# Kernel optimization log

Measured on AMD Instinct MI355X. Metric: run time of the kernel, lower is better.

The kernel has to match this reference:

```python
import jax, jax.numpy as jnp
import numpy as np

D_MODEL = 256
N_HEADS = 8
EPS = 1e-6


def _split_heads(x, h=N_HEADS):
    # (b, n, D) -> (b, h, n, d)
    b, n, D = x.shape
    return x.reshape(b, n, h, D // h).transpose(0, 2, 1, 3)


def _merge_heads(x):
    # (b, h, n, d) -> (b, n, D)
    b, h, n, d = x.shape
    return x.transpose(0, 2, 1, 3).reshape(b, n, h * d)


def _hodge_diag(x, q, k, inv):
    # diagonal discrete Hodge operator: per-position scalar from q.k
    d = q.shape[-1]
    hval = jnp.einsum('bhmd,bhmd->bhm', q, k) / jnp.sqrt(jnp.asarray(d, x.dtype))
    if inv:
        hval = 1.0 / (hval + EPS)
    return hval[..., None] * x


def _forward(x_v, x_e, x_f, d_0, d_1,
             W_vq, W_vk, W_eq, W_ek, W_einvq, W_einvk, W_ev, W_fq, W_fk, W_o):
    # project + split into heads: (b, h, n, d_head)
    v_Q = _split_heads(x_v @ W_vq)
    v_K = _split_heads(x_v @ W_vk)
    e_Q = _split_heads(x_e @ W_eq)
    e_K = _split_heads(x_e @ W_ek)
    e_inv_Q = _split_heads(x_e @ W_einvq)
    e_inv_K = _split_heads(x_e @ W_einvk)
    e_V = _split_heads(x_e @ W_ev)
    f_Q = _split_heads(x_f @ W_fq)
    f_K = _split_heads(x_f @ W_fk)

    # --- up-Laplacian branch: *1^{-1} d_1^T *2 d_1 ---
    _x = e_V
    _x = jnp.einsum('bkm,bhmd->bhkd', d_1, _x)          # d_1 @ x   (edges -> faces)
    _x = _hodge_diag(_x, f_Q, f_K, inv=False)            # *2
    _x = jnp.einsum('bkm,bhkd->bhmd', d_1, _x)           # d_1^T @ x (faces -> edges)
    _x = _hodge_diag(_x, e_inv_Q, e_inv_K, inv=False)    # *1^{-1} (as diag ops, inv=False)

    # --- down-Laplacian branch: d_0 *0^{-1} d_0^T *1 ---
    _y = _hodge_diag(e_V, e_Q, e_K, inv=False)           # *1
    _y = jnp.einsum('bmn,bhmd->bhnd', d_0, _y)           # d_0^T @ y (edges -> vertices)
    _y = _hodge_diag(_y, v_Q, v_K, inv=True)             # *0^{-1} (reciprocal)
    _y = jnp.einsum('bmn,bhnd->bhmd', d_0, _y)           # d_0 @ y  (vertices -> edges)

    out = _merge_heads(_y + _x)                          # (b, m, D)
    return out @ W_o


def setup_inputs() -> dict:
    key = jax.random.key(0)
    ks = jax.random.split(key, 16)
    b, n, m, k, D = 2, 2048, 6144, 4096, D_MODEL
    s = 1.0 / np.sqrt(D)
    inp = {
        'x_v': jax.random.normal(ks[0], (b, n, D), jnp.float32),
        'x_e': jax.random.normal(ks[1], (b, m, D), jnp.float32),
        'x_f': jax.random.normal(ks[2], (b, k, D), jnp.float32),
        'd_0': jax.random.normal(ks[3], (b, m, n), jnp.float32) * 0.02,
        'd_1': jax.random.normal(ks[4], (b, k, m), jnp.float32) * 0.02,
    }
    names = ['W_vq', 'W_vk', 'W_eq', 'W_ek', 'W_einvq', 'W_einvk', 'W_ev', 'W_fq', 'W_fk', 'W_o']
    for i, nm in enumerate(names):
        inp[nm] = jax.random.normal(ks[5 + i], (D, D), jnp.float32) * s
    return inp


def reference(x_v, x_e, x_f, d_0, d_1,
              W_vq, W_vk, W_eq, W_ek, W_einvq, W_einvk, W_ev, W_fq, W_fk, W_o):
    return _forward(x_v, x_e, x_f, d_0, d_1,
                    W_vq, W_vk, W_eq, W_ek, W_einvq, W_einvk, W_ev, W_fq, W_fk, W_o)
```

## Files before the change

### kernel.cpp

```cpp
#include <hip/hip_runtime.h>
#include <hip/hip_bf16.h>
#include <cstdint>
#include <cstddef>


typedef __attribute__((ext_vector_type(4))) float f32x4;
typedef __attribute__((ext_vector_type(4))) unsigned short u16x4;
typedef __attribute__((ext_vector_type(8))) unsigned short u16x8;
typedef __attribute__((ext_vector_type(8))) __bf16 bf16x8;

static __device__ __forceinline__ unsigned short f2bf(float f) {
  uint32_t u = __builtin_bit_cast(uint32_t, f);
  uint32_t r = (u + 0x7FFFu + ((u >> 16) & 1u)) >> 16;
  return (unsigned short)r;
}
static __device__ __forceinline__ float bf2f(unsigned short h) {
  return __builtin_bit_cast(float, (uint32_t)h << 16);
}

struct GJob {
  const unsigned short* Ah; const unsigned short* Bh; float* C;
  int K, ldA, ldB, S, gx, gy;
  long long sA, sB, sC;
};

template <bool XFAST>
__global__ __launch_bounds__(256) void gemm_dual(GJob j0, GJob j1, int nb0) {
  const bool first = (int)blockIdx.x < nb0;
  GJob J = first ? j0 : j1;
  const int b = first ? blockIdx.x : blockIdx.x - nb0;
  const int per = J.gx * J.gy;
  const int z = b / per;
  const int wid = b - z * per;
  const int batch = z / J.S, split = z - batch * J.S;
  const unsigned short* Ah = J.Ah + (long long)batch * J.sA;
  const unsigned short* Bh = J.Bh + (long long)batch * J.sB;
  float* C = J.C + (long long)z * J.sC;

  const int nwg = per;
  const int q = nwg >> 3, r = nwg & 7;
  const int xcd = wid & 7, posn = wid >> 3;
  const int swz = (xcd < r ? xcd * (q + 1) : r * (q + 1) + (xcd - r) * q) + posn;
  int mt, nt;
  if constexpr (XFAST) { mt = swz % J.gx; nt = swz / J.gx; }
  else                 { mt = swz / J.gy; nt = swz - mt * J.gy; }
  const int m0 = mt * 128, n0 = nt * 128;
  const int NC = J.gy << 7;
  const int kLen = J.K / J.S, k0base = split * kLen;

  __shared__ unsigned short lds[2][128][40];

  const int t = threadIdx.x;
  const int w4 = t >> 6, lane = t & 63;
  const int wr = w4 >> 1, wc = w4 & 1;
  const int lr = lane & 15, kq = lane >> 4;
  const int rowV = t >> 2, c8V = (t & 3) * 8;

  u16x8 rA[2], rB[2];
  auto LOAD = [&](int kb) {
    #pragma unroll
    for (int a = 0; a < 2; ++a) {
      rA[a] = *(const u16x8*)(Ah + (size_t)(m0 + rowV + 64 * a) * J.ldA + kb + c8V);
      rB[a] = *(const u16x8*)(Bh + (size_t)(n0 + rowV + 64 * a) * J.ldB + kb + c8V);
    }
  };
  auto STORE = [&]() {
    #pragma unroll
    for (int a = 0; a < 2; ++a) {
      *(u16x8*)&lds[0][rowV + 64 * a][c8V] = rA[a];
      *(u16x8*)&lds[1][rowV + 64 * a][c8V] = rB[a];
    }
  };

  f32x4 acc[4][4] = {};
  LOAD(k0base);
  for (int kk = 0; kk < kLen; kk += 32) {
    STORE();
    __syncthreads();
    if (kk + 32 < kLen) LOAD(k0base + kk + 32);

    bf16x8 ah[4], bh[4];
    #pragma unroll
    for (int i = 0; i < 4; ++i) {
      ah[i] = __builtin_bit_cast(bf16x8, *(const u16x8*)&lds[0][wr * 64 + i * 16 + lr][kq * 8]);
      bh[i] = __builtin_bit_cast(bf16x8, *(const u16x8*)&lds[1][wc * 64 + i * 16 + lr][kq * 8]);
    }
    #pragma unroll
    for (int i = 0; i < 4; ++i)
      #pragma unroll
      for (int j = 0; j < 4; ++j)
        acc[i][j] = __builtin_amdgcn_mfma_f32_16x16x32_bf16(ah[i], bh[j], acc[i][j], 0, 0, 0);
    __syncthreads();
  }

  #pragma unroll
  for (int i = 0; i < 4; ++i)
    #pragma unroll
    for (int j = 0; j < 4; ++j) {
      float* cp = C + (size_t)(m0 + wr * 64 + i * 16 + kq * 4) * NC + n0 + wc * 64 + j * 16 + lr;
      #pragma unroll
      for (int qq = 0; qq < 4; ++qq) cp[(size_t)qq * NC] = acc[i][j][qq];
    }
}

template <bool SPLIT>
__global__ __launch_bounds__(256) void gemm_ws(
    const float* __restrict__ Af,
    const unsigned short* __restrict__ Bh, const unsigned short* __restrict__ Bl,
    float* __restrict__ C, int K, int ldA, int ldB,
    long long sA, long long sB, long long sC) {
  const int gx = gridDim.x, gy = gridDim.y;
  const int nwg = gx * gy;
  const int wid = blockIdx.x + gx * blockIdx.y;
  const int q = nwg >> 3, r = nwg & 7;
  const int xcd = wid & 7, posn = wid >> 3;
  const int swz = (xcd < r ? xcd * (q + 1) : r * (q + 1) + (xcd - r) * q) + posn;
  const int mt = swz / gy;
  const int m0 = mt * 128, n0 = (swz - mt * gy) * 128;
  const int NC = gy << 7;

  constexpr int NBUF = SPLIT ? 4 : 2;
  __shared__ unsigned short lds[NBUF][128][40];

  const int t = threadIdx.x;
  const int w4 = t >> 6, lane = t & 63;
  const int wr = w4 >> 1, wc = w4 & 1;
  const int lr = lane & 15, kq = lane >> 4;
  const int rowA8 = t >> 3, qdA = (t & 7) * 4;
  const int rowV = t >> 2, c8V = (t & 3) * 8;

  f32x4 rAf[4];
  u16x8 rBh[2], rBl[2];

  auto LOAD = [&](int kb) {
    #pragma unroll
    for (int a = 0; a < 4; ++a)
      rAf[a] = *(const f32x4*)(Af + (size_t)(m0 + rowA8 + 32 * a) * ldA + kb + qdA);
    #pragma unroll
    for (int a = 0; a < 2; ++a) {
      rBh[a] = *(const u16x8*)(Bh + (size_t)(n0 + rowV + 64 * a) * ldB + kb + c8V);
      if constexpr (SPLIT)
        rBl[a] = *(const u16x8*)(Bl + (size_t)(n0 + rowV + 64 * a) * ldB + kb + c8V);
    }
  };
  auto STORE = [&]() {
    #pragma unroll
    for (int a = 0; a < 4; ++a) {
      f32x4 v = rAf[a];
      u16x4 h = {f2bf(v[0]), f2bf(v[1]), f2bf(v[2]), f2bf(v[3])};
      *(u16x4*)&lds[0][rowA8 + 32 * a][qdA] = h;
      if constexpr (SPLIT) {
        u16x4 l = {f2bf(v[0] - bf2f(h[0])), f2bf(v[1] - bf2f(h[1])),
                   f2bf(v[2] - bf2f(h[2])), f2bf(v[3] - bf2f(h[3]))};
        *(u16x4*)&lds[2][rowA8 + 32 * a][qdA] = l;
      }
    }
    #pragma unroll
    for (int a = 0; a < 2; ++a) {
      *(u16x8*)&lds[1][rowV + 64 * a][c8V] = rBh[a];
      if constexpr (SPLIT) *(u16x8*)&lds[3][rowV + 64 * a][c8V] = rBl[a];
    }
  };

  f32x4 acc[4][4] = {};
  LOAD(0);
  for (int kk = 0; kk < K; kk += 32) {
    STORE();
    __syncthreads();
    if (kk + 32 < K) LOAD(kk + 32);

    bf16x8 ah[4], bh[4], al[4], bl[4];
    #pragma unroll
    for (int i = 0; i < 4; ++i) {
      ah[i] = __builtin_bit_cast(bf16x8, *(const u16x8*)&lds[0][wr * 64 + i * 16 + lr][kq * 8]);
      bh[i] = __builtin_bit_cast(bf16x8, *(const u16x8*)&lds[1][wc * 64 + i * 16 + lr][kq * 8]);
      if constexpr (SPLIT) {
        al[i] = __builtin_bit_cast(bf16x8, *(const u16x8*)&lds[2][wr * 64 + i * 16 + lr][kq * 8]);
        bl[i] = __builtin_bit_cast(bf16x8, *(const u16x8*)&lds[3][wc * 64 + i * 16 + lr][kq * 8]);
      }
    }
    #pragma unroll
    for (int i = 0; i < 4; ++i)
      #pragma unroll
      for (int j = 0; j < 4; ++j) {
        acc[i][j] = __builtin_amdgcn_mfma_f32_16x16x32_bf16(ah[i], bh[j], acc[i][j], 0, 0, 0);
        if constexpr (SPLIT) {
          acc[i][j] = __builtin_amdgcn_mfma_f32_16x16x32_bf16(ah[i], bl[j], acc[i][j], 0, 0, 0);
          acc[i][j] = __builtin_amdgcn_mfma_f32_16x16x32_bf16(al[i], bh[j], acc[i][j], 0, 0, 0);
        }
      }
    __syncthreads();
  }

  #pragma unroll
  for (int i = 0; i < 4; ++i)
    #pragma unroll
    for (int j = 0; j < 4; ++j) {
      float* cp = C + (size_t)(m0 + wr * 64 + i * 16 + kq * 4) * NC + n0 + wc * 64 + j * 16 + lr;
      #pragma unroll
      for (int qq = 0; qq < 4; ++qq) cp[(size_t)qq * NC] = acc[i][j][qq];
    }
}

__global__ __launch_bounds__(256) void gemm_out(
    const float* __restrict__ T2p, const float* __restrict__ T4p,
    const float* __restrict__ hEi, const unsigned short* __restrict__ Bh,
    const unsigned short* __restrict__ Bl, float* __restrict__ C) {
  const int gx = gridDim.x, gy = gridDim.y;
  const int nwg = gx * gy;
  const int wid = blockIdx.x + gx * blockIdx.y;
  const int q = nwg >> 3, r = nwg & 7;
  const int xcd = wid & 7, posn = wid >> 3;
  const int swz = (xcd < r ? xcd * (q + 1) : r * (q + 1) + (xcd - r) * q) + posn;
  const int mt = swz / gy;
  const int m0 = mt * 128, n0 = (swz - mt * gy) * 128;

  __shared__ unsigned short lds[4][128][40];
  const int t = threadIdx.x;
  const int w4 = t >> 6, lane = t & 63;
  const int wr = w4 >> 1, wc = w4 & 1;
  const int lr = lane & 15, kq = lane >> 4;
  const long long slab = 6144LL * 256;

  f32x4 acc[4][4] = {};

  for (int kb = 0; kb < 256; kb += 32) {
    #pragma unroll
    for (int a = 0; a < 4; ++a) {
      int idx = t + 256 * a;
      int row = idx >> 3, qd = (idx & 7) * 4;
      int rg = m0 + row;
      int b = rg >= 6144;
      int pos = rg - b * 6144;
      int ck = kb + qd;
      float s = hEi[((size_t)b * 8 + (ck >> 5)) * 6144 + pos];
      const float* b2 = T2p + ((long long)(b * 4) * 6144 + pos) * 256 + ck;
      const float* b4 = T4p + ((long long)(b * 4) * 6144 + pos) * 256 + ck;
      f32x4 t2 = (*(const f32x4*)b2 + *(const f32x4*)(b2 + slab)) +
                 (*(const f32x4*)(b2 + 2 * slab) + *(const f32x4*)(b2 + 3 * slab));
      f32x4 t4 = (*(const f32x4*)b4 + *(const f32x4*)(b4 + slab)) +
                 (*(const f32x4*)(b4 + 2 * slab) + *(const f32x4*)(b4 + 3 * slab));
      f32x4 v = t4 + t2 * s;
      u16x4 h = {f2bf(v[0]), f2bf(v[1]), f2bf(v[2]), f2bf(v[3])};
      *(u16x4*)&lds[0][row][qd] = h;
      u16x4 l = {f2bf(v[0] - bf2f(h[0])), f2bf(v[1] - bf2f(h[1])),
                 f2bf(v[2] - bf2f(h[2])), f2bf(v[3] - bf2f(h[3]))};
      *(u16x4*)&lds[2][row][qd] = l;
    }
    #pragma unroll
    for (int a = 0; a < 2; ++a) {
      int idx = t + 256 * a;
      int row = idx >> 2, c8 = (idx & 3) * 8;
      *(u16x8*)&lds[1][row][c8] = *(const u16x8*)(Bh + (size_t)(n0 + row) * 256 + kb + c8);
      *(u16x8*)&lds[3][row][c8] = *(const u16x8*)(Bl + (size_t)(n0 + row) * 256 + kb + c8);
    }
    __syncthreads();

    bf16x8 ah[4], bh[4], al[4], bl[4];
    #pragma unroll
    for (int i = 0; i < 4; ++i) {
      ah[i] = __builtin_bit_cast(bf16x8, *(const u16x8*)&lds[0][wr * 64 + i * 16 + lr][kq * 8]);
      bh[i] = __builtin_bit_cast(bf16x8, *(const u16x8*)&lds[1][wc * 64 + i * 16 + lr][kq * 8]);
      al[i] = __builtin_bit_cast(bf16x8, *(const u16x8*)&lds[2][wr * 64 + i * 16 + lr][kq * 8]);
      bl[i] = __builtin_bit_cast(bf16x8, *(const u16x8*)&lds[3][wc * 64 + i * 16 + lr][kq * 8]);
    }
    #pragma unroll
    for (int i = 0; i < 4; ++i)
      #pragma unroll
      for (int j = 0; j < 4; ++j) {
        acc[i][j] = __builtin_amdgcn_mfma_f32_16x16x32_bf16(ah[i], bh[j], acc[i][j], 0, 0, 0);
        acc[i][j] = __builtin_amdgcn_mfma_f32_16x16x32_bf16(ah[i], bl[j], acc[i][j], 0, 0, 0);
        acc[i][j] = __builtin_amdgcn_mfma_f32_16x16x32_bf16(al[i], bh[j], acc[i][j], 0, 0, 0);
      }
    __syncthreads();
  }

  #pragma unroll
  for (int i = 0; i < 4; ++i)
    #pragma unroll
    for (int j = 0; j < 4; ++j) {
      float* cp = C + (size_t)(m0 + wr * 64 + i * 16 + kq * 4) * 256 + n0 + wc * 64 + j * 16 + lr;
      #pragma unroll
      for (int qq = 0; qq < 4; ++qq) cp[(size_t)qq * 256] = acc[i][j][qq];
    }
}

struct PrepArgs {
  const float* wsrc[8]; unsigned short* wh[8]; unsigned short* wl[8];
  const float* d1; unsigned short* d1T; unsigned short* d1N;
  const float* d0; unsigned short* d0T_hi; unsigned short* d0N_hi;
  const float* xv; const float* Wvq; const float* Wvk; float* hvV;
};

__global__ __launch_bounds__(256) void prep_all(PrepArgs A) {
  __shared__ __align__(16) char smem[24576];
  const int t = threadIdx.x;
  const int bid = blockIdx.x;

  if (bid < 512) {
    float* sx = (float*)smem;
    float* sq = (float*)(smem + 8192);
    float* sk = (float*)(smem + 16384);
    const int r0 = bid * 8;
    const int j = t;
    #pragma unroll
    for (int r = 0; r < 8; ++r) sx[r * 256 + j] = A.xv[(size_t)(r0 + r) * 256 + j];
    __syncthreads();
    float qa[8] = {}, ka[8] = {};
    for (int i = 0; i < 256; ++i) {
      float wq = A.Wvq[i * 256 + j], wk = A.Wvk[i * 256 + j];
      #pragma unroll
      for (int r = 0; r < 8; ++r) {
        qa[r] = __fmaf_rn(sx[r * 256 + i], wq, qa[r]);
        ka[r] = __fmaf_rn(sx[r * 256 + i], wk, ka[r]);
      }
    }
    #pragma unroll
    for (int r = 0; r < 8; ++r) { sq[r * 256 + j] = qa[r]; sk[r * 256 + j] = ka[r]; }
    __syncthreads();
    if (j < 64) {
      const int r = j >> 3, head = j & 7;
      const float* qq = &sq[r * 256 + head * 32];
      const float* kk = &sk[r * 256 + head * 32];
      float s0 = 0.0f, s1 = 0.0f, s2 = 0.0f, s3 = 0.0f;
      #pragma unroll 1
      for (int d = 0; d < 32; d += 4) {
        s0 = __fadd_rn(s0, __fmul_rn(qq[d + 0], kk[d + 0]));
        s1 = __fadd_rn(s1, __fmul_rn(qq[d + 1], kk[d + 1]));
        s2 = __fadd_rn(s2, __fmul_rn(qq[d + 2], kk[d + 2]));
        s3 = __fadd_rn(s3, __fmul_rn(qq[d + 3], kk[d + 3]));
      }
      float p = __fadd_rn(__fadd_rn(s0, s2), __fadd_rn(s1, s3));
      float hval = __fdiv_rn(p, sqrtf(32.0f));
      float inv = __fdiv_rn(1.0f, __fadd_rn(hval, 1e-6f));
      const int row = r0 + r;
      const int b = row / 2048, pos = row - b * 2048;
      A.hvV[((size_t)b * 8 + head) * 2048 + pos] = inv;
    }
  } else if (bid < 640) {
    const int idx = bid - 512;
    const int w = idx >> 4;
    const int r0 = (idx & 3) * 64, c0 = ((idx >> 2) & 3) * 64;
    const float* src = A.wsrc[w];
    unsigned short* oh = A.wh[w];
    unsigned short* ol = A.wl[w];
    unsigned short (*thi)[72] = (unsigned short (*)[72])smem;
    unsigned short (*tlo)[72] = (unsigned short (*)[72])(smem + 9216);
    #pragma unroll
    for (int a = 0; a < 4; ++a) {
      int idx2 = t + 256 * a;
      int tr = idx2 >> 4, tc = (idx2 & 15) * 4;
      f32x4 v = *(const f32x4*)(src + (size_t)(r0 + tr) * 256 + c0 + tc);
      u16x4 hh = {f2bf(v[0]), f2bf(v[1]), f2bf(v[2]), f2bf(v[3])};
      *(u16x4*)&thi[tr][tc] = hh;
      if (ol) {
        u16x4 ll = {f2bf(v[0] - bf2f(hh[0])), f2bf(v[1] - bf2f(hh[1])),
                    f2bf(v[2] - bf2f(hh[2])), f2bf(v[3] - bf2f(hh[3]))};
        *(u16x4*)&tlo[tr][tc] = ll;
      }
    }
    __syncthreads();
    #pragma unroll
    for (int a = 0; a < 2; ++a) {
      int idx2 = t + 256 * a;
      int orow = idx2 >> 3, oc = (idx2 & 7) * 8;
      u16x8 vh;
      #pragma unroll
      for (int j = 0; j < 8; ++j) vh[j] = thi[oc + j][orow];
      *(u16x8*)(oh + (size_t)(c0 + orow) * 256 + r0 + oc) = vh;
      if (ol) {
        u16x8 vl;
        #pragma unroll
        for (int j = 0; j < 8; ++j) vl[j] = tlo[oc + j][orow];
        *(u16x8*)(ol + (size_t)(c0 + orow) * 256 + r0 + oc) = vl;
      }
    }
  } else if (bid < 12928) {
    const int idx = bid - 640;
    const int x = idx & 63;
    const int rem = idx >> 6;
    const int y = rem % 96;
    const int b = rem / 96;
    const int r0 = x * 64, c0 = y * 64;
    unsigned short (*thi)[72] = (unsigned short (*)[72])smem;
    #pragma unroll
    for (int a = 0; a < 4; ++a) {
      int idx2 = t + 256 * a;
      int tr = idx2 >> 4, tc = (idx2 & 15) * 4;
      size_t off = ((size_t)b * 4096 + r0 + tr) * 6144 + c0 + tc;
      f32x4 v = *(const f32x4*)(A.d1 + off);
      u16x4 hh = {f2bf(v[0]), f2bf(v[1]), f2bf(v[2]), f2bf(v[3])};
      *(u16x4*)&thi[tr][tc] = hh;
      *(u16x4*)(A.d1N + off) = hh;
    }
    __syncthreads();
    #pragma unroll
    for (int a = 0; a < 2; ++a) {
      int idx2 = t + 256 * a;
      int orow = idx2 >> 3, oc = (idx2 & 7) * 8;
      u16x8 vh;
      #pragma unroll
      for (int j = 0; j < 8; ++j) vh[j] = thi[oc + j][orow];
      *(u16x8*)(A.d1T + ((size_t)b * 6144 + c0 + orow) * 4096 + r0 + oc) = vh;
    }
  } else {
    const int idx = bid - 12928;
    const int x = idx % 96;
    const int rem = idx / 96;
    const int y = rem & 31;
    const int b = rem >> 5;
    const int r0 = x * 64, c0 = y * 64;
    unsigned short (*thi)[72] = (unsigned short (*)[72])smem;
    #pragma unroll
    for (int a = 0; a < 4; ++a) {
      int idx2 = t + 256 * a;
      int tr = idx2 >> 4, tc = (idx2 & 15) * 4;
      size_t off = ((size_t)b * 6144 + r0 + tr) * 2048 + c0 + tc;
      f32x4 v = *(const f32x4*)(A.d0 + off);
      u16x4 hh = {f2bf(v[0]), f2bf(v[1]), f2bf(v[2]), f2bf(v[3])};
      *(u16x4*)&thi[tr][tc] = hh;
      *(u16x4*)(A.d0N_hi + off) = hh;
    }
    __syncthreads();
    #pragma unroll
    for (int a = 0; a < 2; ++a) {
      int idx2 = t + 256 * a;
      int orow = idx2 >> 3, oc = (idx2 & 7) * 8;
      u16x8 vh;
      #pragma unroll
      for (int j = 0; j < 8; ++j) vh[j] = thi[oc + j][orow];
      *(u16x8*)(A.d0T_hi + ((size_t)b * 2048 + c0 + orow) * 6144 + r0 + oc) = vh;
    }
  }
}

__global__ __launch_bounds__(256) void xpose_ev(
    const float* __restrict__ P1, unsigned short* __restrict__ eVT,
    unsigned short* __restrict__ yhi, const float* __restrict__ hE) {
  __shared__ unsigned short te[64][72], th[64][72];
  const int b = blockIdx.z;
  const int r0 = blockIdx.x * 64, c0 = blockIdx.y * 64;
  const int t = threadIdx.x;
  #pragma unroll
  for (int a = 0; a < 4; ++a) {
    int idx = t + 256 * a;
    int tr = idx >> 4, tc = (idx & 15) * 4;
    f32x4 v = *(const f32x4*)(P1 + ((size_t)b * 6144 + r0 + tr) * 1280 + 512 + c0 + tc);
    u16x4 eh = {f2bf(v[0]), f2bf(v[1]), f2bf(v[2]), f2bf(v[3])};
    *(u16x4*)&te[tr][tc] = eh;
    float s = hE[((size_t)b * 8 + ((c0 + tc) >> 5)) * 6144 + r0 + tr];
    f32x4 y = v * s;
    u16x4 hh = {f2bf(y[0]), f2bf(y[1]), f2bf(y[2]), f2bf(y[3])};
    *(u16x4*)&th[tr][tc] = hh;
  }
  __syncthreads();
  #pragma unroll
  for (int a = 0; a < 2; ++a) {
    int idx = t + 256 * a;
    int orow = idx >> 3, oc = (idx & 7) * 8;
    u16x8 ve, vh;
    #pragma unroll
    for (int j = 0; j < 8; ++j) {
      ve[j] = te[oc + j][orow];
      vh[j] = th[oc + j][orow];
    }
    size_t o = ((size_t)b * 256 + c0 + orow) * 6144 + r0 + oc;
    *(u16x8*)(eVT + o) = ve;
    *(u16x8*)(yhi + o) = vh;
  }
}

static __device__ __forceinline__ void rsc_body(
    const float* in, unsigned short* out_hi, const float* h,
    int S, int R, int P, int bid, int nblk) {
  const long long qP = P >> 2;
  const long long nq = 2LL * R * qP;
  long long i = (long long)bid * 256 + threadIdx.x;
  const long long stride = (long long)nblk * 256;
  for (; i < nq; i += stride) {
    long long b = i / (R * qP);
    long long rem = i - b * (R * qP);
    int row = (int)(rem / qP);
    long long qc = rem - (long long)row * qP;
    const f32x4* base = (const f32x4*)in + ((b * S) * R + row) * qP + qc;
    f32x4 v = base[0];
    for (int s = 1; s < S; ++s) v += base[(long long)s * R * qP];
    v *= *(const f32x4*)(h + ((size_t)b * 8 + (row >> 5)) * P + (qc << 2));
    u16x4 hh = {f2bf(v[0]), f2bf(v[1]), f2bf(v[2]), f2bf(v[3])};
    ((u16x4*)out_hi)[i] = hh;
  }
}

__global__ void rsc2(const float* in1, unsigned short* o1h, const float* hF,
                     const float* in3, unsigned short* o3h, const float* hV) {
  if (blockIdx.x < 2048)
    rsc_body(in1, o1h, hF, 6, 256, 4096, blockIdx.x, 2048);
  else
    rsc_body(in3, o3h, hV, 12, 256, 2048, blockIdx.x - 2048, 1024);
}

__global__ __launch_bounds__(256) void dots(
    const float* __restrict__ P1, float* __restrict__ hE, float* __restrict__ hEi,
    const float* __restrict__ P3, float* __restrict__ hF) {
  const int wv = threadIdx.x >> 6, lane = threadIdx.x & 63;
  if (blockIdx.x < 3072) {
    const int row = blockIdx.x * 4 + wv;
    const float* base = P1 + (size_t)row * 1280 + lane * 4;
    f32x4 qv = *(const f32x4*)(base);
    f32x4 kv = *(const f32x4*)(base + 256);
    float p = qv[0] * kv[0] + qv[1] * kv[1] + qv[2] * kv[2] + qv[3] * kv[3];
    p += __shfl_xor(p, 1); p += __shfl_xor(p, 2); p += __shfl_xor(p, 4);
    f32x4 q2 = *(const f32x4*)(base + 768);
    f32x4 k2 = *(const f32x4*)(base + 1024);
    float p2 = q2[0] * k2[0] + q2[1] * k2[1] + q2[2] * k2[2] + q2[3] * k2[3];
    p2 += __shfl_xor(p2, 1); p2 += __shfl_xor(p2, 2); p2 += __shfl_xor(p2, 4);
    if ((lane & 7) == 0) {
      const int head = lane >> 3;
      const int b = row / 6144, pos = row % 6144;
      hE[((size_t)b * 8 + head) * 6144 + pos] = p * 0.17677669529663687f;
      hEi[((size_t)b * 8 + head) * 6144 + pos] = p2 * 0.17677669529663687f;
    }
  } else {
    const int row = (blockIdx.x - 3072) * 4 + wv;
    const float* base = P3 + (size_t)row * 512 + lane * 4;
    f32x4 qv = *(const f32x4*)(base);
    f32x4 kv = *(const f32x4*)(base + 256);
    float p = qv[0] * kv[0] + qv[1] * kv[1] + qv[2] * kv[2] + qv[3] * kv[3];
    p += __shfl_xor(p, 1); p += __shfl_xor(p, 2); p += __shfl_xor(p, 4);
    if ((lane & 7) == 0) {
      const int head = lane >> 3;
      const int b = row / 4096, pos = row % 4096;
      hF[((size_t)b * 8 + head) * 4096 + pos] = p * 0.17677669529663687f;
    }
  }
}

extern "C" void kernel_launch(void* const* d_in, const int* in_sizes, int n_in,
                              void* d_out, int out_size, void* d_ws, size_t ws_size,
                              hipStream_t stream) {
  const float* x_v = (const float*)d_in[0];
  const float* x_e = (const float*)d_in[1];
  const float* x_f = (const float*)d_in[2];
  const float* d0  = (const float*)d_in[3];
  const float* d1  = (const float*)d_in[4];
  float* out = (float*)d_out;

  const int NV = 2048, ME = 6144, KF = 4096;
  const unsigned short* NUS = nullptr;

  char* ws = (char*)d_ws;
  size_t o = 0;
  auto alloc = [&](size_t bytes) { size_t r = o; o = (o + bytes + 255) & ~255ULL; return r; };

  unsigned short* Wcat5_hi = (unsigned short*)(ws + alloc(1280 * 256 * 2));
  unsigned short* Wcat5_lo = (unsigned short*)(ws + alloc(1280 * 256 * 2));
  unsigned short* W3_hi = (unsigned short*)(ws + alloc(512 * 256 * 2));
  unsigned short* Wo_hi = (unsigned short*)(ws + alloc(256 * 256 * 2));
  unsigned short* Wo_lo = (unsigned short*)(ws + alloc(256 * 256 * 2));
  float* pHvE  = (float*)(ws + alloc(2 * 8 * ME * 4));
  float* pHvEi = (float*)(ws + alloc(2 * 8 * ME * 4));
  float* pHvF  = (float*)(ws + alloc(2 * 8 * KF * 4));
  float* pHvV  = (float*)(ws + alloc(2 * 8 * NV * 4));
  unsigned short* d1T_hi = (unsigned short*)(ws + alloc((size_t)2 * ME * KF * 2));
  unsigned short* d1N_hi = (unsigned short*)(ws + alloc((size_t)2 * KF * ME * 2));
  unsigned short* d0T_hi = (unsigned short*)(ws + alloc((size_t)2 * NV * ME * 2));
  unsigned short* d0N_hi = (unsigned short*)(ws + alloc((size_t)2 * ME * NV * 2));
  unsigned short* eVT_hi = (unsigned short*)(ws + alloc((size_t)2 * 256 * ME * 2));
  unsigned short* Y0T_hi = (unsigned short*)(ws + alloc((size_t)2 * 256 * ME * 2));
  unsigned short* T1sT_hi = (unsigned short*)(ws + alloc((size_t)2 * 256 * KF * 2));
  unsigned short* T3sT_hi = (unsigned short*)(ws + alloc((size_t)2 * 256 * NV * 2));
  float* pP1 = (float*)(ws + alloc((size_t)12288 * 1280 * 4));
  float* pP3 = (float*)(ws + alloc((size_t)8192 * 512 * 4));
  float* pTp1 = (float*)(ws + alloc((size_t)2 * 6 * 256 * KF * 4));
  float* pTp3 = (float*)(ws + alloc((size_t)2 * 12 * 256 * NV * 4));
  float* pT2p = (float*)(ws + alloc((size_t)2 * 4 * ME * 256 * 4));
  float* pT4p = (float*)(ws + alloc((size_t)2 * 4 * ME * 256 * 4));

  dim3 blk(256);

  PrepArgs pa;
  pa.wsrc[0] = (const float*)d_in[7];  pa.wh[0] = Wcat5_hi;          pa.wl[0] = Wcat5_lo;
  pa.wsrc[1] = (const float*)d_in[8];  pa.wh[1] = Wcat5_hi + 65536;  pa.wl[1] = Wcat5_lo + 65536;
  pa.wsrc[2] = (const float*)d_in[11]; pa.wh[2] = Wcat5_hi + 131072; pa.wl[2] = Wcat5_lo + 131072;
  pa.wsrc[3] = (const float*)d_in[9];  pa.wh[3] = Wcat5_hi + 196608; pa.wl[3] = Wcat5_lo + 196608;
  pa.wsrc[4] = (const float*)d_in[10]; pa.wh[4] = Wcat5_hi + 262144; pa.wl[4] = Wcat5_lo + 262144;
  pa.wsrc[5] = (const float*)d_in[12]; pa.wh[5] = W3_hi;             pa.wl[5] = nullptr;
  pa.wsrc[6] = (const float*)d_in[13]; pa.wh[6] = W3_hi + 65536;     pa.wl[6] = nullptr;
  pa.wsrc[7] = (const float*)d_in[14]; pa.wh[7] = Wo_hi;             pa.wl[7] = Wo_lo;
  pa.d1 = d1; pa.d1T = d1T_hi; pa.d1N = d1N_hi;
  pa.d0 = d0; pa.d0T_hi = d0T_hi; pa.d0N_hi = d0N_hi;
  pa.xv = x_v; pa.Wvq = (const float*)d_in[5]; pa.Wvk = (const float*)d_in[6];
  pa.hvV = pHvV;
  prep_all<<<19072, blk, 0, stream>>>(pa);

  gemm_ws<true><<<dim3(96, 10, 1), blk, 0, stream>>>(
      x_e, Wcat5_hi, Wcat5_lo, pP1, 256, 256, 256, 0, 0, 0);
  gemm_ws<false><<<dim3(64, 4, 1), blk, 0, stream>>>(
      x_f, W3_hi, NUS, pP3, 256, 256, 256, 0, 0, 0);
  dots<<<5120, blk, 0, stream>>>(pP1, pHvE, pHvEi, pP3, pHvF);
  xpose_ev<<<dim3(96, 4, 2), blk, 0, stream>>>(pP1, eVT_hi, Y0T_hi, pHvE);

  GJob jT1, jT3;
  jT1.Ah = eVT_hi; jT1.Bh = d1N_hi; jT1.C = pTp1;
  jT1.K = ME; jT1.ldA = ME; jT1.ldB = ME; jT1.S = 6; jT1.gx = 2; jT1.gy = 32;
  jT1.sA = 256LL * ME; jT1.sB = (long long)KF * ME; jT1.sC = 256LL * KF;
  jT3.Ah = Y0T_hi; jT3.Bh = d0T_hi; jT3.C = pTp3;
  jT3.K = ME; jT3.ldA = ME; jT3.ldB = ME; jT3.S = 12; jT3.gx = 2; jT3.gy = 16;
  jT3.sA = 256LL * ME; jT3.sB = (long long)NV * ME; jT3.sC = 256LL * NV;
  gemm_dual<true><<<1536, blk, 0, stream>>>(jT1, jT3, 768);

  rsc2<<<3072, blk, 0, stream>>>(pTp1, T1sT_hi, pHvF, pTp3, T3sT_hi, pHvV);

  GJob jT2, jT4;
  jT2.Ah = d1T_hi; jT2.Bh = T1sT_hi; jT2.C = pT2p;
  jT2.K = KF; jT2.ldA = KF; jT2.ldB = KF; jT2.S = 4; jT2.gx = 48; jT2.gy = 2;
  jT2.sA = (long long)ME * KF; jT2.sB = 256LL * KF; jT2.sC = (long long)ME * 256;
  jT4.Ah = d0N_hi; jT4.Bh = T3sT_hi; jT4.C = pT4p;
  jT4.K = NV; jT4.ldA = NV; jT4.ldB = NV; jT4.S = 4; jT4.gx = 48; jT4.gy = 2;
  jT4.sA = (long long)ME * NV; jT4.sB = 256LL * NV; jT4.sC = (long long)ME * 256;
  gemm_dual<false><<<1536, blk, 0, stream>>>(jT2, jT4, 768);

  gemm_out<<<dim3(96, 2, 1), blk, 0, stream>>>(pT2p, pT4p, pHvEi, Wo_hi, Wo_lo, out);
}
```

Measured before the change: 431.1 us.

## Fuse projection GEMMs into prep megakernel and halve split-K factors

Moves the weight transpose into its own small kernel and folds the two projection GEMMs (x_e and x_f) into the big prep kernel, so they run alongside the d0/d1 conversion and the vertex Hodge work. This removes two kernel launches and their serialization gaps. Separately, it halves the split-K factors of the four big incidence GEMMs (6→3, 12→6, 4→2). That cuts partial-sum traffic and the reduction work in rsc2 and gemm_out, but launches fewer workgroups with longer K loops. The projection GEMMs in the megakernel now depend on the weights being converted by the preceding wxpose launch.

```diff
diff --git a/kernel.cpp b/kernel.cpp
--- a/kernel.cpp
+++ b/kernel.cpp
@@ -104,14 +104,12 @@
 }
 
 template <bool SPLIT>
-__global__ __launch_bounds__(256) void gemm_ws(
-    const float* __restrict__ Af,
-    const unsigned short* __restrict__ Bh, const unsigned short* __restrict__ Bl,
-    float* __restrict__ C, int K, int ldA, int ldB,
-    long long sA, long long sB, long long sC) {
-  const int gx = gridDim.x, gy = gridDim.y;
+static __device__ void proj_gemm(char* smem, int wid, int gx, int gy,
+                                 const float* __restrict__ Af,
+                                 const unsigned short* __restrict__ Bh,
+                                 const unsigned short* __restrict__ Bl,
+                                 float* __restrict__ C) {
   const int nwg = gx * gy;
-  const int wid = blockIdx.x + gx * blockIdx.y;
   const int q = nwg >> 3, r = nwg & 7;
   const int xcd = wid & 7, posn = wid >> 3;
   const int swz = (xcd < r ? xcd * (q + 1) : r * (q + 1) + (xcd - r) * q) + posn;
@@ -119,8 +117,8 @@
   const int m0 = mt * 128, n0 = (swz - mt * gy) * 128;
   const int NC = gy << 7;
 
-  constexpr int NBUF = SPLIT ? 4 : 2;
-  __shared__ unsigned short lds[NBUF][128][40];
+  typedef unsigned short ldsrow[128][40];
+  ldsrow* lds = (ldsrow*)smem;
 
   const int t = threadIdx.x;
   const int w4 = t >> 6, lane = t & 63;
@@ -135,12 +133,12 @@
   auto LOAD = [&](int kb) {
     #pragma unroll
     for (int a = 0; a < 4; ++a)
-      rAf[a] = *(const f32x4*)(Af + (size_t)(m0 + rowA8 + 32 * a) * ldA + kb + qdA);
+      rAf[a] = *(const f32x4*)(Af + (size_t)(m0 + rowA8 + 32 * a) * 256 + kb + qdA);
     #pragma unroll
     for (int a = 0; a < 2; ++a) {
-      rBh[a] = *(const u16x8*)(Bh + (size_t)(n0 + rowV + 64 * a) * ldB + kb + c8V);
+      rBh[a] = *(const u16x8*)(Bh + (size_t)(n0 + rowV + 64 * a) * 256 + kb + c8V);
       if constexpr (SPLIT)
-        rBl[a] = *(const u16x8*)(Bl + (size_t)(n0 + rowV + 64 * a) * ldB + kb + c8V);
+        rBl[a] = *(const u16x8*)(Bl + (size_t)(n0 + rowV + 64 * a) * 256 + kb + c8V);
     }
   };
   auto STORE = [&]() {
@@ -164,10 +162,10 @@
 
   f32x4 acc[4][4] = {};
   LOAD(0);
-  for (int kk = 0; kk < K; kk += 32) {
+  for (int kk = 0; kk < 256; kk += 32) {
     STORE();
     __syncthreads();
-    if (kk + 32 < K) LOAD(kk + 32);
+    if (kk + 32 < 256) LOAD(kk + 32);
 
     bf16x8 ah[4], bh[4], al[4], bl[4];
     #pragma unroll
@@ -202,106 +200,30 @@
     }
 }
 
-__global__ __launch_bounds__(256) void gemm_out(
-    const float* __restrict__ T2p, const float* __restrict__ T4p,
-    const float* __restrict__ hEi, const unsigned short* __restrict__ Bh,
-    const unsigned short* __restrict__ Bl, float* __restrict__ C) {
-  const int gx = gridDim.x, gy = gridDim.y;
-  const int nwg = gx * gy;
-  const int wid = blockIdx.x + gx * blockIdx.y;
-  const int q = nwg >> 3, r = nwg & 7;
-  const int xcd = wid & 7, posn = wid >> 3;
-  const int swz = (xcd < r ? xcd * (q + 1) : r * (q + 1) + (xcd - r) * q) + posn;
-  const int mt = swz / gy;
-  const int m0 = mt * 128, n0 = (swz - mt * gy) * 128;
-
-  __shared__ unsigned short lds[4][128][40];
-  const int t = threadIdx.x;
-  const int w4 = t >> 6, lane = t & 63;
-  const int wr = w4 >> 1, wc = w4 & 1;
-  const int lr = lane & 15, kq = lane >> 4;
-  const long long slab = 6144LL * 256;
-
-  f32x4 acc[4][4] = {};
-
-  for (int kb = 0; kb < 256; kb += 32) {
-    #pragma unroll
-    for (int a = 0; a < 4; ++a) {
-      int idx = t + 256 * a;
-      int row = idx >> 3, qd = (idx & 7) * 4;
-      int rg = m0 + row;
-      int b = rg >= 6144;
-      int pos = rg - b * 6144;
-      int ck = kb + qd;
-      float s = hEi[((size_t)b * 8 + (ck >> 5)) * 6144 + pos];
-      const float* b2 = T2p + ((long long)(b * 4) * 6144 + pos) * 256 + ck;
-      const float* b4 = T4p + ((long long)(b * 4) * 6144 + pos) * 256 + ck;
-      f32x4 t2 = (*(const f32x4*)b2 + *(const f32x4*)(b2 + slab)) +
-                 (*(const f32x4*)(b2 + 2 * slab) + *(const f32x4*)(b2 + 3 * slab));
-      f32x4 t4 = (*(const f32x4*)b4 + *(const f32x4*)(b4 + slab)) +
-                 (*(const f32x4*)(b4 + 2 * slab) + *(const f32x4*)(b4 + 3 * slab));
-      f32x4 v = t4 + t2 * s;
-      u16x4 h = {f2bf(v[0]), f2bf(v[1]), f2bf(v[2]), f2bf(v[3])};
-      *(u16x4*)&lds[0][row][qd] = h;
-      u16x4 l = {f2bf(v[0] - bf2f(h[0])), f2bf(v[1] - bf2f(h[1])),
-                 f2bf(v[2] - bf2f(h[2])), f2bf(v[3] - bf2f(h[3]))};
-      *(u16x4*)&lds[2][row][qd] = l;
-    }
-    #pragma unroll
-    for (int a = 0; a < 2; ++a) {
-      int idx = t + 256 * a;
-      int row = idx >> 2, c8 = (idx & 3) * 8;
-      *(u16x8*)&lds[1][row][c8] = *(const u16x8*)(Bh + (size_t)(n0 + row) * 256 + kb + c8);
-      *(u16x8*)&lds[3][row][c8] = *(const u16x8*)(Bl + (size_t)(n0 + row) * 256 + kb + c8);
-    }
-    __syncthreads();
-
-    bf16x8 ah[4], bh[4], al[4], bl[4];
-    #pragma unroll
-    for (int i = 0; i < 4; ++i) {
-      ah[i] = __builtin_bit_cast(bf16x8, *(const u16x8*)&lds[0][wr * 64 + i * 16 + lr][kq * 8]);
-      bh[i] = __builtin_bit_cast(bf16x8, *(const u16x8*)&lds[1][wc * 64 + i * 16 + lr][kq * 8]);
-      al[i] = __builtin_bit_cast(bf16x8, *(const u16x8*)&lds[2][wr * 64 + i * 16 + lr][kq * 8]);
-      bl[i] = __builtin_bit_cast(bf16x8, *(const u16x8*)&lds[3][wc * 64 + i * 16 + lr][kq * 8]);
-    }
-    #pragma unroll
-    for (int i = 0; i < 4; ++i)
-      #pragma unroll
-      for (int j = 0; j < 4; ++j) {
-        acc[i][j] = __builtin_amdgcn_mfma_f32_16x16x32_bf16(ah[i], bh[j], acc[i][j], 0, 0, 0);
-        acc[i][j] = __builtin_amdgcn_mfma_f32_16x16x32_bf16(ah[i], bl[j], acc[i][j], 0, 0, 0);
-        acc[i][j] = __builtin_amdgcn_mfma_f32_16x16x32_bf16(al[i], bh[j], acc[i][j], 0, 0, 0);
-      }
-    __syncthreads();
-  }
-
-  #pragma unroll
-  for (int i = 0; i < 4; ++i)
-    #pragma unroll
-    for (int j = 0; j < 4; ++j) {
-      float* cp = C + (size_t)(m0 + wr * 64 + i * 16 + kq * 4) * 256 + n0 + wc * 64 + j * 16 + lr;
-      #pragma unroll
-      for (int qq = 0; qq < 4; ++qq) cp[(size_t)qq * 256] = acc[i][j][qq];
-    }
-}
-
-struct PrepArgs {
-  const float* wsrc[8]; unsigned short* wh[8]; unsigned short* wl[8];
+struct MegaArgs {
+  const float* xe; const float* xf;
+  const unsigned short* Wcat5_hi; const unsigned short* Wcat5_lo;
+  const unsigned short* W3_hi;
+  float* P1; float* P3;
+  const float* xv; const float* Wvq; const float* Wvk; float* hvV;
   const float* d1; unsigned short* d1T; unsigned short* d1N;
-  const float* d0; unsigned short* d0T_hi; unsigned short* d0N_hi;
-  const float* xv; const float* Wvq; const float* Wvk; float* hvV;
+  const float* d0; unsigned short* d0T; unsigned short* d0N;
 };
 
-__global__ __launch_bounds__(256) void prep_all(PrepArgs A) {
-  __shared__ __align__(16) char smem[24576];
+__global__ __launch_bounds__(256) void mega2(MegaArgs A) {
+  __shared__ __align__(16) char smem[40960];
   const int t = threadIdx.x;
   const int bid = blockIdx.x;
 
-  if (bid < 512) {
+  if (bid < 960) {
+    proj_gemm<true>(smem, bid, 96, 10, A.xe, A.Wcat5_hi, A.Wcat5_lo, A.P1);
+  } else if (bid < 1216) {
+    proj_gemm<false>(smem, bid - 960, 64, 4, A.xf, A.W3_hi, nullptr, A.P3);
+  } else if (bid < 1728) {
     float* sx = (float*)smem;
     float* sq = (float*)(smem + 8192);
     float* sk = (float*)(smem + 16384);
-    const int r0 = bid * 8;
+    const int r0 = (bid - 1216) * 8;
     const int j = t;
     #pragma unroll
     for (int r = 0; r < 8; ++r) sx[r * 256 + j] = A.xv[(size_t)(r0 + r) * 256 + j];
@@ -337,46 +259,8 @@
       const int b = row / 2048, pos = row - b * 2048;
       A.hvV[((size_t)b * 8 + head) * 2048 + pos] = inv;
     }
-  } else if (bid < 640) {
-    const int idx = bid - 512;
-    const int w = idx >> 4;
-    const int r0 = (idx & 3) * 64, c0 = ((idx >> 2) & 3) * 64;
-    const float* src = A.wsrc[w];
-    unsigned short* oh = A.wh[w];
-    unsigned short* ol = A.wl[w];
-    unsigned short (*thi)[72] = (unsigned short (*)[72])smem;
-    unsigned short (*tlo)[72] = (unsigned short (*)[72])(smem + 9216);
-    #pragma unroll
-    for (int a = 0; a < 4; ++a) {
-      int idx2 = t + 256 * a;
-      int tr = idx2 >> 4, tc = (idx2 & 15) * 4;
-      f32x4 v = *(const f32x4*)(src + (size_t)(r0 + tr) * 256 + c0 + tc);
-      u16x4 hh = {f2bf(v[0]), f2bf(v[1]), f2bf(v[2]), f2bf(v[3])};
-      *(u16x4*)&thi[tr][tc] = hh;
-      if (ol) {
-        u16x4 ll = {f2bf(v[0] - bf2f(hh[0])), f2bf(v[1] - bf2f(hh[1])),
-                    f2bf(v[2] - bf2f(hh[2])), f2bf(v[3] - bf2f(hh[3]))};
-        *(u16x4*)&tlo[tr][tc] = ll;
-      }
-    }
-    __syncthreads();
-    #pragma unroll
-    for (int a = 0; a < 2; ++a) {
-      int idx2 = t + 256 * a;
-      int orow = idx2 >> 3, oc = (idx2 & 7) * 8;
-      u16x8 vh;
-      #pragma unroll
-      for (int j = 0; j < 8; ++j) vh[j] = thi[oc + j][orow];
-      *(u16x8*)(oh + (size_t)(c0 + orow) * 256 + r0 + oc) = vh;
-      if (ol) {
-        u16x8 vl;
-        #pragma unroll
-        for (int j = 0; j < 8; ++j) vl[j] = tlo[oc + j][orow];
-        *(u16x8*)(ol + (size_t)(c0 + orow) * 256 + r0 + oc) = vl;
-      }
-    }
-  } else if (bid < 12928) {
-    const int idx = bid - 640;
+  } else if (bid < 14016) {
+    const int idx = bid - 1728;
     const int x = idx & 63;
     const int rem = idx >> 6;
     const int y = rem % 96;
@@ -404,7 +288,7 @@
       *(u16x8*)(A.d1T + ((size_t)b * 6144 + c0 + orow) * 4096 + r0 + oc) = vh;
     }
   } else {
-    const int idx = bid - 12928;
+    const int idx = bid - 14016;
     const int x = idx % 96;
     const int rem = idx / 96;
     const int y = rem & 31;
@@ -419,7 +303,7 @@
       f32x4 v = *(const f32x4*)(A.d0 + off);
       u16x4 hh = {f2bf(v[0]), f2bf(v[1]), f2bf(v[2]), f2bf(v[3])};
       *(u16x4*)&thi[tr][tc] = hh;
-      *(u16x4*)(A.d0N_hi + off) = hh;
+      *(u16x4*)(A.d0N + off) = hh;
     }
     __syncthreads();
     #pragma unroll
@@ -429,7 +313,132 @@
       u16x8 vh;
       #pragma unroll
       for (int j = 0; j < 8; ++j) vh[j] = thi[oc + j][orow];
-      *(u16x8*)(A.d0T_hi + ((size_t)b * 2048 + c0 + orow) * 6144 + r0 + oc) = vh;
+      *(u16x8*)(A.d0T + ((size_t)b * 2048 + c0 + orow) * 6144 + r0 + oc) = vh;
+    }
+  }
+}
+
+__global__ __launch_bounds__(256) void gemm_out(
+    const float* __restrict__ T2p, const float* __restrict__ T4p,
+    const float* __restrict__ hEi, const unsigned short* __restrict__ Bh,
+    const unsigned short* __restrict__ Bl, float* __restrict__ C) {
+  const int gx = gridDim.x, gy = gridDim.y;
+  const int nwg = gx * gy;
+  const int wid = blockIdx.x + gx * blockIdx.y;
+  const int q = nwg >> 3, r = nwg & 7;
+  const int xcd = wid & 7, posn = wid >> 3;
+  const int swz = (xcd < r ? xcd * (q + 1) : r * (q + 1) + (xcd - r) * q) + posn;
+  const int mt = swz / gy;
+  const int m0 = mt * 128, n0 = (swz - mt * gy) * 128;
+
+  __shared__ unsigned short lds[4][128][40];
+  const int t = threadIdx.x;
+  const int w4 = t >> 6, lane = t & 63;
+  const int wr = w4 >> 1, wc = w4 & 1;
+  const int lr = lane & 15, kq = lane >> 4;
+  const long long slab = 6144LL * 256;
+
+  f32x4 acc[4][4] = {};
+
+  for (int kb = 0; kb < 256; kb += 32) {
+    #pragma unroll
+    for (int a = 0; a < 4; ++a) {
+      int idx = t + 256 * a;
+      int row = idx >> 3, qd = (idx & 7) * 4;
+      int rg = m0 + row;
+      int b = rg >= 6144;
+      int pos = rg - b * 6144;
+      int ck = kb + qd;
+      float s = hEi[((size_t)b * 8 + (ck >> 5)) * 6144 + pos];
+      const float* b2 = T2p + ((long long)(b * 2) * 6144 + pos) * 256 + ck;
+      const float* b4 = T4p + ((long long)(b * 2) * 6144 + pos) * 256 + ck;
+      f32x4 t2 = *(const f32x4*)b2 + *(const f32x4*)(b2 + slab);
+      f32x4 t4 = *(const f32x4*)b4 + *(const f32x4*)(b4 + slab);
+      f32x4 v = t4 + t2 * s;
+      u16x4 h = {f2bf(v[0]), f2bf(v[1]), f2bf(v[2]), f2bf(v[3])};
+      *(u16x4*)&lds[0][row][qd] = h;
+      u16x4 l = {f2bf(v[0] - bf2f(h[0])), f2bf(v[1] - bf2f(h[1])),
+                 f2bf(v[2] - bf2f(h[2])), f2bf(v[3] - bf2f(h[3]))};
+      *(u16x4*)&lds[2][row][qd] = l;
+    }
+    #pragma unroll
+    for (int a = 0; a < 2; ++a) {
+      int idx = t + 256 * a;
+      int row = idx >> 2, c8 = (idx & 3) * 8;
+      *(u16x8*)&lds[1][row][c8] = *(const u16x8*)(Bh + (size_t)(n0 + row) * 256 + kb + c8);
+      *(u16x8*)&lds[3][row][c8] = *(const u16x8*)(Bl + (size_t)(n0 + row) * 256 + kb + c8);
+    }
+    __syncthreads();
+
+    bf16x8 ah[4], bh[4], al[4], bl[4];
+    #pragma unroll
+    for (int i = 0; i < 4; ++i) {
+      ah[i] = __builtin_bit_cast(bf16x8, *(const u16x8*)&lds[0][wr * 64 + i * 16 + lr][kq * 8]);
+      bh[i] = __builtin_bit_cast(bf16x8, *(const u16x8*)&lds[1][wc * 64 + i * 16 + lr][kq * 8]);
+      al[i] = __builtin_bit_cast(bf16x8, *(const u16x8*)&lds[2][wr * 64 + i * 16 + lr][kq * 8]);
+      bl[i] = __builtin_bit_cast(bf16x8, *(const u16x8*)&lds[3][wc * 64 + i * 16 + lr][kq * 8]);
+    }
+    #pragma unroll
+    for (int i = 0; i < 4; ++i)
+      #pragma unroll
+      for (int j = 0; j < 4; ++j) {
+        acc[i][j] = __builtin_amdgcn_mfma_f32_16x16x32_bf16(ah[i], bh[j], acc[i][j], 0, 0, 0);
+        acc[i][j] = __builtin_amdgcn_mfma_f32_16x16x32_bf16(ah[i], bl[j], acc[i][j], 0, 0, 0);
+        acc[i][j] = __builtin_amdgcn_mfma_f32_16x16x32_bf16(al[i], bh[j], acc[i][j], 0, 0, 0);
+      }
+    __syncthreads();
+  }
+
+  #pragma unroll
+  for (int i = 0; i < 4; ++i)
+    #pragma unroll
+    for (int j = 0; j < 4; ++j) {
+      float* cp = C + (size_t)(m0 + wr * 64 + i * 16 + kq * 4) * 256 + n0 + wc * 64 + j * 16 + lr;
+      #pragma unroll
+      for (int qq = 0; qq < 4; ++qq) cp[(size_t)qq * 256] = acc[i][j][qq];
+    }
+}
+
+struct WTab {
+  const float* s[8];
+  unsigned short* h[8];
+  unsigned short* l[8];
+};
+__global__ __launch_bounds__(256) void wxpose(WTab tab) {
+  __shared__ unsigned short thi[64][72], tlo[64][72];
+  const int w = blockIdx.z;
+  const float* src = tab.s[w];
+  unsigned short* oh = tab.h[w];
+  unsigned short* ol = tab.l[w];
+  const int r0 = blockIdx.x * 64, c0 = blockIdx.y * 64;
+  const int t = threadIdx.x;
+  #pragma unroll
+  for (int a = 0; a < 4; ++a) {
+    int idx = t + 256 * a;
+    int tr = idx >> 4, tc = (idx & 15) * 4;
+    f32x4 v = *(const f32x4*)(src + (size_t)(r0 + tr) * 256 + c0 + tc);
+    u16x4 hh = {f2bf(v[0]), f2bf(v[1]), f2bf(v[2]), f2bf(v[3])};
+    *(u16x4*)&thi[tr][tc] = hh;
+    if (ol) {
+      u16x4 ll = {f2bf(v[0] - bf2f(hh[0])), f2bf(v[1] - bf2f(hh[1])),
+                  f2bf(v[2] - bf2f(hh[2])), f2bf(v[3] - bf2f(hh[3]))};
+      *(u16x4*)&tlo[tr][tc] = ll;
+    }
+  }
+  __syncthreads();
+  #pragma unroll
+  for (int a = 0; a < 2; ++a) {
+    int idx = t + 256 * a;
+    int orow = idx >> 3, oc = (idx & 7) * 8;
+    u16x8 vh;
+    #pragma unroll
+    for (int j = 0; j < 8; ++j) vh[j] = thi[oc + j][orow];
+    *(u16x8*)(oh + (size_t)(c0 + orow) * 256 + r0 + oc) = vh;
+    if (ol) {
+      u16x8 vl;
+      #pragma unroll
+      for (int j = 0; j < 8; ++j) vl[j] = tlo[oc + j][orow];
+      *(u16x8*)(ol + (size_t)(c0 + orow) * 256 + r0 + oc) = vl;
     }
   }
 }
@@ -494,9 +503,9 @@
 __global__ void rsc2(const float* in1, unsigned short* o1h, const float* hF,
                      const float* in3, unsigned short* o3h, const float* hV) {
   if (blockIdx.x < 2048)
-    rsc_body(in1, o1h, hF, 6, 256, 4096, blockIdx.x, 2048);
+    rsc_body(in1, o1h, hF, 3, 256, 4096, blockIdx.x, 2048);
   else
-    rsc_body(in3, o3h, hV, 12, 256, 2048, blockIdx.x - 2048, 1024);
+    rsc_body(in3, o3h, hV, 6, 256, 2048, blockIdx.x - 2048, 1024);
 }
 
 __global__ __launch_bounds__(256) void dots(
@@ -546,7 +555,6 @@
   float* out = (float*)d_out;
 
   const int NV = 2048, ME = 6144, KF = 4096;
-  const unsigned short* NUS = nullptr;
 
   char* ws = (char*)d_ws;
   size_t o = 0;
@@ -571,54 +579,56 @@
   unsigned short* T3sT_hi = (unsigned short*)(ws + alloc((size_t)2 * 256 * NV * 2));
   float* pP1 = (float*)(ws + alloc((size_t)12288 * 1280 * 4));
   float* pP3 = (float*)(ws + alloc((size_t)8192 * 512 * 4));
-  float* pTp1 = (float*)(ws + alloc((size_t)2 * 6 * 256 * KF * 4));
-  float* pTp3 = (float*)(ws + alloc((size_t)2 * 12 * 256 * NV * 4));
-  float* pT2p = (float*)(ws + alloc((size_t)2 * 4 * ME * 256 * 4));
-  float* pT4p = (float*)(ws + alloc((size_t)2 * 4 * ME * 256 * 4));
+  float* pTp1 = (float*)(ws + alloc((size_t)2 * 3 * 256 * KF * 4));
+  float* pTp3 = (float*)(ws + alloc((size_t)2 * 6 * 256 * NV * 4));
+  float* pT2p = (float*)(ws + alloc((size_t)2 * 2 * ME * 256 * 4));
+  float* pT4p = (float*)(ws + alloc((size_t)2 * 2 * ME * 256 * 4));
 
   dim3 blk(256);
 
-  PrepArgs pa;
-  pa.wsrc[0] = (const float*)d_in[7];  pa.wh[0] = Wcat5_hi;          pa.wl[0] = Wcat5_lo;
-  pa.wsrc[1] = (const float*)d_in[8];  pa.wh[1] = Wcat5_hi + 65536;  pa.wl[1] = Wcat5_lo + 65536;
-  pa.wsrc[2] = (const float*)d_in[11]; pa.wh[2] = Wcat5_hi + 131072; pa.wl[2] = Wcat5_lo + 131072;
-  pa.wsrc[3] = (const float*)d_in[9];  pa.wh[3] = Wcat5_hi + 196608; pa.wl[3] = Wcat5_lo + 196608;
-  pa.wsrc[4] = (const float*)d_in[10]; pa.wh[4] = Wcat5_hi + 262144; pa.wl[4] = Wcat5_lo + 262144;
-  pa.wsrc[5] = (const float*)d_in[12]; pa.wh[5] = W3_hi;             pa.wl[5] = nullptr;
-  pa.wsrc[6] = (const float*)d_in[13]; pa.wh[6] = W3_hi + 65536;     pa.wl[6] = nullptr;
-  pa.wsrc[7] = (const float*)d_in[14]; pa.wh[7] = Wo_hi;             pa.wl[7] = Wo_lo;
-  pa.d1 = d1; pa.d1T = d1T_hi; pa.d1N = d1N_hi;
-  pa.d0 = d0; pa.d0T_hi = d0T_hi; pa.d0N_hi = d0N_hi;
-  pa.xv = x_v; pa.Wvq = (const float*)d_in[5]; pa.Wvk = (const float*)d_in[6];
-  pa.hvV = pHvV;
-  prep_all<<<19072, blk, 0, stream>>>(pa);
-
-  gemm_ws<true><<<dim3(96, 10, 1), blk, 0, stream>>>(
-      x_e, Wcat5_hi, Wcat5_lo, pP1, 256, 256, 256, 0, 0, 0);
-  gemm_ws<false><<<dim3(64, 4, 1), blk, 0, stream>>>(
-      x_f, W3_hi, NUS, pP3, 256, 256, 256, 0, 0, 0);
+  WTab tab;
+  tab.s[0] = (const float*)d_in[7];  tab.h[0] = Wcat5_hi;          tab.l[0] = Wcat5_lo;
+  tab.s[1] = (const float*)d_in[8];  tab.h[1] = Wcat5_hi + 65536;  tab.l[1] = Wcat5_lo + 65536;
+  tab.s[2] = (const float*)d_in[11]; tab.h[2] = Wcat5_hi + 131072; tab.l[2] = Wcat5_lo + 131072;
+  tab.s[3] = (const float*)d_in[9];  tab.h[3] = Wcat5_hi + 196608; tab.l[3] = Wcat5_lo + 196608;
+  tab.s[4] = (const float*)d_in[10]; tab.h[4] = Wcat5_hi + 262144; tab.l[4] = Wcat5_lo + 262144;
+  tab.s[5] = (const float*)d_in[12]; tab.h[5] = W3_hi;             tab.l[5] = nullptr;
+  tab.s[6] = (const float*)d_in[13]; tab.h[6] = W3_hi + 65536;     tab.l[6] = nullptr;
+  tab.s[7] = (const float*)d_in[14]; tab.h[7] = Wo_hi;             tab.l[7] = Wo_lo;
+  wxpose<<<dim3(4, 4, 8), blk, 0, stream>>>(tab);
+
+  MegaArgs ma;
+  ma.xe = x_e; ma.xf = x_f;
+  ma.Wcat5_hi = Wcat5_hi; ma.Wcat5_lo = Wcat5_lo; ma.W3_hi = W3_hi;
+  ma.P1 = pP1; ma.P3 = pP3;
+  ma.xv = x_v; ma.Wvq = (const float*)d_in[5]; ma.Wvk = (const float*)d_in[6];
+  ma.hvV = pHvV;
+  ma.d1 = d1; ma.d1T = d1T_hi; ma.d1N = d1N_hi;
+  ma.d0 = d0; ma.d0T = d0T_hi; ma.d0N = d0N_hi;
+  mega2<<<20160, blk, 0, stream>>>(ma);
+
   dots<<<5120, blk, 0, stream>>>(pP1, pHvE, pHvEi, pP3, pHvF);
   xpose_ev<<<dim3(96, 4, 2), blk, 0, stream>>>(pP1, eVT_hi, Y0T_hi, pHvE);
 
   GJob jT1, jT3;
   jT1.Ah = eVT_hi; jT1.Bh = d1N_hi; jT1.C = pTp1;
-  jT1.K = ME; jT1.ldA = ME; jT1.ldB = ME; jT1.S = 6; jT1.gx = 2; jT1.gy = 32;
+  jT1.K = ME; jT1.ldA = ME; jT1.ldB = ME; jT1.S = 3; jT1.gx = 2; jT1.gy = 32;
   jT1.sA = 256LL * ME; jT1.sB = (long long)KF * ME; jT1.sC = 256LL * KF;
   jT3.Ah = Y0T_hi; jT3.Bh = d0T_hi; jT3.C = pTp3;
-  jT3.K = ME; jT3.ldA = ME; jT3.ldB = ME; jT3.S = 12; jT3.gx = 2; jT3.gy = 16;
+  jT3.K = ME; jT3.ldA = ME; jT3.ldB = ME; jT3.S = 6; jT3.gx = 2; jT3.gy = 16;
   jT3.sA = 256LL * ME; jT3.sB = (long long)NV * ME; jT3.sC = 256LL * NV;
-  gemm_dual<true><<<1536, blk, 0, stream>>>(jT1, jT3, 768);
+  gemm_dual<true><<<768, blk, 0, stream>>>(jT1, jT3, 384);
 
   rsc2<<<3072, blk, 0, stream>>>(pTp1, T1sT_hi, pHvF, pTp3, T3sT_hi, pHvV);
 
   GJob jT2, jT4;
   jT2.Ah = d1T_hi; jT2.Bh = T1sT_hi; jT2.C = pT2p;
-  jT2.K = KF; jT2.ldA = KF; jT2.ldB = KF; jT2.S = 4; jT2.gx = 48; jT2.gy = 2;
+  jT2.K = KF; jT2.ldA = KF; jT2.ldB = KF; jT2.S = 2; jT2.gx = 48; jT2.gy = 2;
   jT2.sA = (long long)ME * KF; jT2.sB = 256LL * KF; jT2.sC = (long long)ME * 256;
   jT4.Ah = d0N_hi; jT4.Bh = T3sT_hi; jT4.C = pT4p;
-  jT4.K = NV; jT4.ldA = NV; jT4.ldB = NV; jT4.S = 4; jT4.gx = 48; jT4.gy = 2;
+  jT4.K = NV; jT4.ldA = NV; jT4.ldB = NV; jT4.S = 2; jT4.gx = 48; jT4.gy = 2;
   jT4.sA = (long long)ME * NV; jT4.sB = 256LL * NV; jT4.sC = (long long)ME * 256;
-  gemm_dual<false><<<1536, blk, 0, stream>>>(jT2, jT4, 768);
+  gemm_dual<false><<<768, blk, 0, stream>>>(jT2, jT4, 384);
 
   gemm_out<<<dim3(96, 2, 1), blk, 0, stream>>>(pT2p, pT4p, pHvEi, Wo_hi, Wo_lo, out);
 }
```

Result: slower. 474.7 us (+10.1%).
